# Kernel tuning notes

Measured on AMD Instinct MI355X. Metric: run time of the kernel, lower is better.

## Reference

```python
import jax, jax.numpy as jnp
import numpy as np


def count_sketch(x, h, s, output_dim):
    # x: [B, d], h: [d] int bucket indices, s: [d] +/-1 signs
    # one nonzero per input feature -> scatter-add into output columns
    return jnp.zeros((x.shape[0], output_dim), dtype=x.dtype).at[:, h].add(x * s)


def setup_inputs() -> dict:
    key = jax.random.key(0)
    k1, k2, k3, k4 = jax.random.split(key, 4)
    B, d, D = 2048, 2048, 16000
    img_vec = jax.random.normal(k1, (B, d), dtype=jnp.float32)
    seq_vec = jax.random.normal(k2, (B, d), dtype=jnp.float32)
    h_vec = jax.random.randint(k3, (d,), 0, D, dtype=jnp.int32)
    # random +/-1 signs (count-sketch s vector)
    s_vec = jnp.where(jax.random.bernoulli(k4, 0.5, (d,)), 1.0, -1.0).astype(jnp.float32)
    return {"img_vec": img_vec, "seq_vec": seq_vec, "h_vec": h_vec, "s_vec": s_vec, "output_dim": D}


def reference(img_vec, seq_vec, h_vec, s_vec, output_dim):
    sk_img = count_sketch(img_vec, h_vec, s_vec, output_dim)  # [B, D]
    sk_seq = count_sketch(seq_vec, h_vec, s_vec, output_dim)  # [B, D]
    # circular convolution of the two sketches via FFT (complex64)
    fft_img = jnp.fft.fft(sk_img)
    fft_seq = jnp.fft.fft(sk_seq)
    out = jnp.fft.ifft(fft_img * fft_seq)
    return jnp.real(out).astype(img_vec.dtype)
```

## Files before the change

kernel.cpp:

```cpp
#include <hip/hip_runtime.h>
#include <math.h>

#define NFFT  16000
#define NCCOL 125
#define DFEAT 2048
#define TPB   1024
#define R2OFF 16000
#define R5OFF 16064
#define LDSN  16189

__device__ __forceinline__ float2 cmul(float2 a, float2 b) {
    return make_float2(a.x*b.x - a.y*b.y, a.x*b.y + a.y*b.x);
}
__device__ __forceinline__ float2 cmulc(float2 a, float2 b) {
    return make_float2(a.x*b.x + a.y*b.y, a.y*b.x - a.x*b.y);
}
__device__ __forceinline__ float2 cadd(float2 a, float2 b){ return make_float2(a.x+b.x, a.y+b.y); }
__device__ __forceinline__ float2 csub(float2 a, float2 b){ return make_float2(a.x-b.x, a.y-b.y); }
__device__ __forceinline__ float2 eipi(float a) {
    float s, c;
    sincospif(a, &s, &c);
    return make_float2(c, s);
}

#define C1f 0.30901699437494742f
#define C2f (-0.80901699437494745f)
#define S1f 0.95105651629515357f
#define S2f 0.58778525229247314f

__device__ __forceinline__ void bfly5_fwd(float2& e0, float2& e1, float2& e2,
                                          float2& e3, float2& e4) {
    float2 t1 = cadd(e1, e4), t2 = cadd(e2, e3);
    float2 t3 = csub(e1, e4), t4 = csub(e2, e3);
    float2 f0 = make_float2(e0.x + t1.x + t2.x, e0.y + t1.y + t2.y);
    float2 m1 = make_float2(e0.x + C1f*t1.x + C2f*t2.x, e0.y + C1f*t1.y + C2f*t2.y);
    float2 m2 = make_float2(e0.x + C2f*t1.x + C1f*t2.x, e0.y + C2f*t1.y + C1f*t2.y);
    float2 v1 = make_float2(S1f*t3.x + S2f*t4.x, S1f*t3.y + S2f*t4.y);
    float2 v2 = make_float2(S2f*t3.x - S1f*t4.x, S2f*t3.y - S1f*t4.y);
    e0 = f0;
    e1 = make_float2(m1.x + v1.y, m1.y - v1.x);
    e4 = make_float2(m1.x - v1.y, m1.y + v1.x);
    e2 = make_float2(m2.x + v2.y, m2.y - v2.x);
    e3 = make_float2(m2.x - v2.y, m2.y + v2.x);
}
__device__ __forceinline__ void bfly5_inv(float2& e0, float2& e1, float2& e2,
                                          float2& e3, float2& e4) {
    float2 t1 = cadd(e1, e4), t2 = cadd(e2, e3);
    float2 t3 = csub(e1, e4), t4 = csub(e2, e3);
    float2 f0 = make_float2(e0.x + t1.x + t2.x, e0.y + t1.y + t2.y);
    float2 m1 = make_float2(e0.x + C1f*t1.x + C2f*t2.x, e0.y + C1f*t1.y + C2f*t2.y);
    float2 m2 = make_float2(e0.x + C2f*t1.x + C1f*t2.x, e0.y + C2f*t1.y + C1f*t2.y);
    float2 v1 = make_float2(S1f*t3.x + S2f*t4.x, S1f*t3.y + S2f*t4.y);
    float2 v2 = make_float2(S2f*t3.x - S1f*t4.x, S2f*t3.y - S1f*t4.y);
    e0 = f0;
    e1 = make_float2(m1.x - v1.y, m1.y + v1.x);
    e4 = make_float2(m1.x + v1.y, m1.y - v1.x);
    e2 = make_float2(m2.x - v2.y, m2.y + v2.x);
    e3 = make_float2(m2.x + v2.y, m2.y - v2.x);
}

__global__ void fill_cross_lut(float2* __restrict__ ws) {
    int p = blockIdx.x * 256 + threadIdx.x;
    if (p < NFFT) {
        int r  = p / NCCOL;
        int c  = p - r * NCCOL;
        int k1 = __brev((unsigned)r) >> 25;
        ws[p]  = eipi((float)(c * k1) * (-2.0f / (float)NFFT));
    }
}

__global__ void __launch_bounds__(TPB) __attribute__((amdgpu_waves_per_eu(4, 4)))
mcb_fft_conv_kernel(const float* __restrict__ img, const float* __restrict__ seq,
                    const int* __restrict__ hvec, const float* __restrict__ svec,
                    float* __restrict__ out, const float2* __restrict__ cross)
{
    extern __shared__ float2 buf[];
    const int tid = threadIdx.x;
    const int b   = blockIdx.x;

    #define W2L(k) buf[R2OFF + (k)]
    #define R5L(k) buf[R5OFF + (k)]

    auto CW = [&](int p) -> float2 {
        if (cross) return cross[p];
        int r = p / NCCOL, c = p - r * NCCOL;
        int k1 = __brev((unsigned)r) >> 25;
        return eipi((float)(c * k1) * (-2.0f / (float)NFFT));
    };

    {
        float4* b4 = (float4*)buf;
        for (int p = tid; p < NFFT / 2; p += TPB) b4[p] = make_float4(0.f, 0.f, 0.f, 0.f);
    }
    if (tid < 64) {
        W2L(tid) = eipi(-(float)tid * (1.0f / 64.0f));
    } else if (tid < 64 + 125) {
        int k = tid - 64;
        R5L(k) = eipi((float)k * (-2.0f / 125.0f));
    }
    __syncthreads();

    {
        const float* irow = img + (size_t)b * DFEAT;
        const float* qrow = seq + (size_t)b * DFEAT;
        for (int j = tid; j < DFEAT; j += TPB) {
            float sj = svec[j];
            int   hj = hvec[j];
            atomicAdd(&buf[hj].x, irow[j] * sj);
            atomicAdd(&buf[hj].y, qrow[j] * sj);
        }
    }
    __syncthreads();

    for (int idx = tid; idx < 16 * NCCOL; idx += TPB) {
        const int j = idx / NCCOL;
        const int c = idx - j * NCCOL;
        const int base = j * NCCOL + c;
        float2 x[8];
        #pragma unroll
        for (int t = 0; t < 8; ++t) x[t] = buf[base + 2000 * t];
        #pragma unroll
        for (int t = 0; t < 4; ++t) {
            float2 u = x[t], v = x[t+4];
            x[t]   = cadd(u, v);
            x[t+4] = cmul(csub(u, v), W2L(j + 16*t));
        }
        #pragma unroll
        for (int q = 0; q < 8; q += 4)
            #pragma unroll
            for (int t = 0; t < 2; ++t) {
                float2 u = x[q+t], v = x[q+t+2];
                x[q+t]   = cadd(u, v);
                x[q+t+2] = cmul(csub(u, v), W2L(2*(j + 16*t)));
            }
        {
            float2 w = W2L(4*j);
            #pragma unroll
            for (int q = 0; q < 8; q += 2) {
                float2 u = x[q], v = x[q+1];
                x[q]   = cadd(u, v);
                x[q+1] = cmul(csub(u, v), w);
            }
        }
        #pragma unroll
        for (int t = 0; t < 8; ++t) buf[base + 2000 * t] = x[t];
    }
    __syncthreads();

    for (int idx = tid; idx < 8 * NCCOL; idx += TPB) {
        const int g = idx / NCCOL;
        const int c = idx - g * NCCOL;
        const int base = 2000 * g + c;
        float2 x[16];
        #pragma unroll
        for (int t = 0; t < 16; ++t) x[t] = buf[base + 125 * t];
        #pragma unroll
        for (int t = 0; t < 8; ++t) {
            float2 u = x[t], v = x[t+8];
            x[t]   = cadd(u, v);
            x[t+8] = cmul(csub(u, v), W2L(8*t));
        }
        #pragma unroll
        for (int q = 0; q < 16; q += 8)
            #pragma unroll
            for (int t = 0; t < 4; ++t) {
                float2 u = x[q+t], v = x[q+t+4];
                x[q+t]   = cadd(u, v);
                x[q+t+4] = cmul(csub(u, v), W2L(16*t));
            }
        #pragma unroll
        for (int q = 0; q < 16; q += 4)
            #pragma unroll
            for (int t = 0; t < 2; ++t) {
                float2 u = x[q+t], v = x[q+t+2];
                x[q+t]   = cadd(u, v);
                x[q+t+2] = cmul(csub(u, v), W2L(32*t));
            }
        #pragma unroll
        for (int q = 0; q < 16; q += 2) {
            float2 u = x[q], v = x[q+1];
            x[q]   = cadd(u, v);
            x[q+1] = csub(u, v);
        }
        #pragma unroll
        for (int t = 0; t < 16; ++t)
            buf[base + 125 * t] = cmul(x[t], CW(base + 125 * t));
    }
    __syncthreads();

    for (int idx = tid; idx < 128 * 25; idx += TPB) {
        const int r = idx / 25;
        const int m = idx - r * 25;
        const int base = r * NCCOL + m;
        float2 x0 = buf[base],      x1 = buf[base + 25], x2 = buf[base + 50],
               x3 = buf[base + 75], x4 = buf[base + 100];
        bfly5_fwd(x0, x1, x2, x3, x4);
        x1 = cmul(x1, R5L(m));
        x2 = cmul(x2, R5L(2*m));
        x3 = cmul(x3, R5L(3*m));
        x4 = cmul(x4, R5L(4*m));
        buf[base] = x0; buf[base + 25] = x1; buf[base + 50] = x2;
        buf[base + 75] = x3; buf[base + 100] = x4;
    }
    __syncthreads();

    for (int idx = tid; idx < 128 * 25; idx += TPB) {
        const int r  = idx / 25;
        const int s  = idx - r * 25;
        const int t5 = s / 5;
        const int j2 = s - t5 * 5;
        const int base = r * NCCOL + j2 + 25 * t5;
        float2 x0 = buf[base],      x1 = buf[base + 5],  x2 = buf[base + 10],
               x3 = buf[base + 15], x4 = buf[base + 20];
        bfly5_fwd(x0, x1, x2, x3, x4);
        x1 = cmul(x1, R5L(5*j2));
        x2 = cmul(x2, R5L(10*j2));
        x3 = cmul(x3, R5L(15*j2));
        x4 = cmul(x4, R5L(20*j2));
        buf[base] = x0; buf[base + 5] = x1; buf[base + 10] = x2;
        buf[base + 15] = x3; buf[base + 20] = x4;
    }
    __syncthreads();

    for (int idx = tid; idx < 128 * 25; idx += TPB) {
        const int r = idx / 25;
        const int q = idx - r * 25;
        const int base = r * NCCOL + 5 * q;
        float2 g0 = buf[base], g1 = buf[base+1], g2 = buf[base+2],
               g3 = buf[base+3], g4 = buf[base+4];
        bfly5_fwd(g0, g1, g2, g3, g4);
        g0 = make_float2(g0.x*g0.x - g0.y*g0.y, 2.f*g0.x*g0.y);
        g1 = make_float2(g1.x*g1.x - g1.y*g1.y, 2.f*g1.x*g1.y);
        g2 = make_float2(g2.x*g2.x - g2.y*g2.y, 2.f*g2.x*g2.y);
        g3 = make_float2(g3.x*g3.x - g3.y*g3.y, 2.f*g3.x*g3.y);
        g4 = make_float2(g4.x*g4.x - g4.y*g4.y, 2.f*g4.x*g4.y);
        bfly5_inv(g0, g1, g2, g3, g4);
        buf[base] = g0; buf[base+1] = g1; buf[base+2] = g2;
        buf[base+3] = g3; buf[base+4] = g4;
    }
    __syncthreads();

    for (int idx = tid; idx < 128 * 25; idx += TPB) {
        const int r  = idx / 25;
        const int s  = idx - r * 25;
        const int t5 = s / 5;
        const int j2 = s - t5 * 5;
        const int base = r * NCCOL + j2 + 25 * t5;
        float2 x0 = buf[base],      x1 = buf[base + 5],  x2 = buf[base + 10],
               x3 = buf[base + 15], x4 = buf[base + 20];
        x1 = cmulc(x1, R5L(5*j2));
        x2 = cmulc(x2, R5L(10*j2));
        x3 = cmulc(x3, R5L(15*j2));
        x4 = cmulc(x4, R5L(20*j2));
        bfly5_inv(x0, x1, x2, x3, x4);
        buf[base] = x0; buf[base + 5] = x1; buf[base + 10] = x2;
        buf[base + 15] = x3; buf[base + 20] = x4;
    }
    __syncthreads();

    for (int idx = tid; idx < 128 * 25; idx += TPB) {
        const int r = idx / 25;
        const int m = idx - r * 25;
        const int base = r * NCCOL + m;
        float2 x0 = buf[base],      x1 = buf[base + 25], x2 = buf[base + 50],
               x3 = buf[base + 75], x4 = buf[base + 100];
        x1 = cmulc(x1, R5L(m));
        x2 = cmulc(x2, R5L(2*m));
        x3 = cmulc(x3, R5L(3*m));
        x4 = cmulc(x4, R5L(4*m));
        bfly5_inv(x0, x1, x2, x3, x4);
        buf[base] = x0; buf[base + 25] = x1; buf[base + 50] = x2;
        buf[base + 75] = x3; buf[base + 100] = x4;
    }
    __syncthreads();

    for (int idx = tid; idx < 8 * NCCOL; idx += TPB) {
        const int g = idx / NCCOL;
        const int c = idx - g * NCCOL;
        const int base = 2000 * g + c;
        float2 x[16];
        #pragma unroll
        for (int t = 0; t < 16; ++t)
            x[t] = cmulc(buf[base + 125 * t], CW(base + 125 * t));
        #pragma unroll
        for (int q = 0; q < 16; q += 2) {
            float2 u = x[q], v = x[q+1];
            x[q]   = cadd(u, v);
            x[q+1] = csub(u, v);
        }
        #pragma unroll
        for (int q = 0; q < 16; q += 4)
            #pragma unroll
            for (int t = 0; t < 2; ++t) {
                float2 u = x[q+t];
                float2 v = cmulc(x[q+t+2], W2L(32*t));
                x[q+t]   = cadd(u, v);
                x[q+t+2] = csub(u, v);
            }
        #pragma unroll
        for (int q = 0; q < 16; q += 8)
            #pragma unroll
            for (int t = 0; t < 4; ++t) {
                float2 u = x[q+t];
                float2 v = cmulc(x[q+t+4], W2L(16*t));
                x[q+t]   = cadd(u, v);
                x[q+t+4] = csub(u, v);
            }
        #pragma unroll
        for (int t = 0; t < 8; ++t) {
            float2 u = x[t];
            float2 v = cmulc(x[t+8], W2L(8*t));
            x[t]   = cadd(u, v);
            x[t+8] = csub(u, v);
        }
        #pragma unroll
        for (int t = 0; t < 16; ++t) buf[base + 125 * t] = x[t];
    }
    __syncthreads();

    const float scale = 1.0f / (2.0f * (float)NFFT);
    float* orow = out + (size_t)b * NFFT;
    for (int idx = tid; idx < 16 * NCCOL; idx += TPB) {
        const int j = idx / NCCOL;
        const int c = idx - j * NCCOL;
        const int base = j * NCCOL + c;
        float2 x[8];
        #pragma unroll
        for (int t = 0; t < 8; ++t) x[t] = buf[base + 2000 * t];
        {
            float2 w = W2L(4*j);
            #pragma unroll
            for (int q = 0; q < 8; q += 2) {
                float2 u = x[q];
                float2 v = cmulc(x[q+1], w);
                x[q]   = cadd(u, v);
                x[q+1] = csub(u, v);
            }
        }
        #pragma unroll
        for (int q = 0; q < 8; q += 4)
            #pragma unroll
            for (int t = 0; t < 2; ++t) {
                float2 u = x[q+t];
                float2 v = cmulc(x[q+t+2], W2L(2*(j + 16*t)));
                x[q+t]   = cadd(u, v);
                x[q+t+2] = csub(u, v);
            }
        #pragma unroll
        for (int t = 0; t < 4; ++t) {
            float2 u = x[t];
            float2 v = cmulc(x[t+4], W2L(j + 16*t));
            orow[base + 2000 * t]       = (u.y + v.y) * scale;
            orow[base + 2000 * (t + 4)] = (u.y - v.y) * scale;
        }
    }
}

extern "C" void kernel_launch(void* const* d_in, const int* in_sizes, int n_in,
                              void* d_out, int out_size, void* d_ws, size_t ws_size,
                              hipStream_t stream)
{
    const float* img  = (const float*)d_in[0];
    const float* seq  = (const float*)d_in[1];
    const int*   hvec = (const int*)d_in[2];
    const float* svec = (const float*)d_in[3];
    float* out = (float*)d_out;

    const int B = in_sizes[0] / DFEAT;
    const size_t lds_bytes = (size_t)LDSN * sizeof(float2);

    const bool use_lut = ws_size >= (size_t)NFFT * sizeof(float2);
    float2* cross = use_lut ? (float2*)d_ws : nullptr;
    if (use_lut) {
        hipLaunchKernelGGL(fill_cross_lut, dim3((NFFT + 255) / 256), dim3(256), 0, stream,
                           cross);
    }

    hipFuncSetAttribute((const void*)mcb_fft_conv_kernel,
                        hipFuncAttributeMaxDynamicSharedMemorySize,
                        (int)lds_bytes);

    hipLaunchKernelGGL(mcb_fft_conv_kernel, dim3(B), dim3(TPB), lds_bytes, stream,
                       img, seq, hvec, svec, out, cross);
}
```

Baseline: 371.3 us.

## Pad FFT LDS rows to 132 stride and use power-of-two thread indexing

Changes the shared-memory layout of the 128x125 FFT matrix to a padded row stride of 132, and the cross-twiddle LUT to match. The radix-2 stages now map threads with shifts and masks instead of divisions by 125, run fixed unrolled iteration counts, and the extra padded lanes do dummy work. Scatter-add and output stores are remapped through the padded layout. The aim is to cut integer division cost and change the LDS bank pattern, at the cost of extra LDS footprint (which may affect occupancy) and wasted lanes on padding columns.

```diff
diff --git a/kernel.cpp b/kernel.cpp
--- a/kernel.cpp
+++ b/kernel.cpp
@@ -2,12 +2,15 @@
 #include <math.h>
 
 #define NFFT  16000
+#define NROW  128
 #define NCCOL 125
+#define LDST  132
+#define DATN  (NROW * LDST)
 #define DFEAT 2048
 #define TPB   1024
-#define R2OFF 16000
-#define R5OFF 16064
-#define LDSN  16189
+#define R2OFF DATN
+#define R5OFF (DATN + 64)
+#define LDSN  (DATN + 64 + 125)
 
 __device__ __forceinline__ float2 cmul(float2 a, float2 b) {
     return make_float2(a.x*b.x - a.y*b.y, a.x*b.y + a.y*b.x);
@@ -59,13 +62,17 @@
     e3 = make_float2(m2.x + v2.y, m2.y - v2.x);
 }
 
-__global__ void fill_cross_lut(float2* __restrict__ ws) {
+__global__ void fill_cross_lut_pad(float2* __restrict__ ws) {
     int p = blockIdx.x * 256 + threadIdx.x;
-    if (p < NFFT) {
-        int r  = p / NCCOL;
-        int c  = p - r * NCCOL;
-        int k1 = __brev((unsigned)r) >> 25;
-        ws[p]  = eipi((float)(c * k1) * (-2.0f / (float)NFFT));
+    if (p < DATN) {
+        int r  = p / LDST;
+        int c  = p - r * LDST;
+        float2 v = make_float2(0.f, 0.f);
+        if (c < NCCOL) {
+            int k1 = __brev((unsigned)r) >> 25;
+            v = eipi((float)(c * k1) * (-2.0f / (float)NFFT));
+        }
+        ws[p] = v;
     }
 }
 
@@ -81,16 +88,15 @@
     #define W2L(k) buf[R2OFF + (k)]
     #define R5L(k) buf[R5OFF + (k)]
 
-    auto CW = [&](int p) -> float2 {
-        if (cross) return cross[p];
-        int r = p / NCCOL, c = p - r * NCCOL;
-        int k1 = __brev((unsigned)r) >> 25;
+    auto CW = [&](int row, int c) -> float2 {
+        if (cross) return cross[row * LDST + c];
+        int k1 = __brev((unsigned)row) >> 25;
         return eipi((float)(c * k1) * (-2.0f / (float)NFFT));
     };
 
     {
         float4* b4 = (float4*)buf;
-        for (int p = tid; p < NFFT / 2; p += TPB) b4[p] = make_float4(0.f, 0.f, 0.f, 0.f);
+        for (int p = tid; p < DATN / 2; p += TPB) b4[p] = make_float4(0.f, 0.f, 0.f, 0.f);
     }
     if (tid < 64) {
         W2L(tid) = eipi(-(float)tid * (1.0f / 64.0f));
@@ -103,22 +109,28 @@
     {
         const float* irow = img + (size_t)b * DFEAT;
         const float* qrow = seq + (size_t)b * DFEAT;
-        for (int j = tid; j < DFEAT; j += TPB) {
+        #pragma unroll
+        for (int it = 0; it < DFEAT / TPB; ++it) {
+            const int j = tid + (it << 10);
             float sj = svec[j];
             int   hj = hvec[j];
-            atomicAdd(&buf[hj].x, irow[j] * sj);
-            atomicAdd(&buf[hj].y, qrow[j] * sj);
-        }
-    }
-    __syncthreads();
-
-    for (int idx = tid; idx < 16 * NCCOL; idx += TPB) {
-        const int j = idx / NCCOL;
-        const int c = idx - j * NCCOL;
-        const int base = j * NCCOL + c;
+            int   hr = hj / NCCOL;
+            int   ha = hr * LDST + (hj - hr * NCCOL);
+            atomicAdd(&buf[ha].x, irow[j] * sj);
+            atomicAdd(&buf[ha].y, qrow[j] * sj);
+        }
+    }
+    __syncthreads();
+
+    #pragma unroll
+    for (int it = 0; it < 2; ++it) {
+        const int idx = tid + (it << 10);
+        const int j = idx >> 7;
+        const int c = idx & 127;
+        const int base = j * LDST + c;
         float2 x[8];
         #pragma unroll
-        for (int t = 0; t < 8; ++t) x[t] = buf[base + 2000 * t];
+        for (int t = 0; t < 8; ++t) x[t] = buf[base + 16 * LDST * t];
         #pragma unroll
         for (int t = 0; t < 4; ++t) {
             float2 u = x[t], v = x[t+4];
@@ -143,17 +155,18 @@
             }
         }
         #pragma unroll
-        for (int t = 0; t < 8; ++t) buf[base + 2000 * t] = x[t];
-    }
-    __syncthreads();
-
-    for (int idx = tid; idx < 8 * NCCOL; idx += TPB) {
-        const int g = idx / NCCOL;
-        const int c = idx - g * NCCOL;
-        const int base = 2000 * g + c;
+        for (int t = 0; t < 8; ++t) buf[base + 16 * LDST * t] = x[t];
+    }
+    __syncthreads();
+
+    {
+        const int g = tid >> 7;
+        const int c = tid & 127;
+        const int base = g * (16 * LDST) + c;
+        const int row0 = g << 4;
         float2 x[16];
         #pragma unroll
-        for (int t = 0; t < 16; ++t) x[t] = buf[base + 125 * t];
+        for (int t = 0; t < 16; ++t) x[t] = buf[base + LDST * t];
         #pragma unroll
         for (int t = 0; t < 8; ++t) {
             float2 u = x[t], v = x[t+8];
@@ -184,14 +197,14 @@
         }
         #pragma unroll
         for (int t = 0; t < 16; ++t)
-            buf[base + 125 * t] = cmul(x[t], CW(base + 125 * t));
+            buf[base + LDST * t] = cmul(x[t], CW(row0 + t, c));
     }
     __syncthreads();
 
     for (int idx = tid; idx < 128 * 25; idx += TPB) {
         const int r = idx / 25;
         const int m = idx - r * 25;
-        const int base = r * NCCOL + m;
+        const int base = r * LDST + m;
         float2 x0 = buf[base],      x1 = buf[base + 25], x2 = buf[base + 50],
                x3 = buf[base + 75], x4 = buf[base + 100];
         bfly5_fwd(x0, x1, x2, x3, x4);
@@ -209,7 +222,7 @@
         const int s  = idx - r * 25;
         const int t5 = s / 5;
         const int j2 = s - t5 * 5;
-        const int base = r * NCCOL + j2 + 25 * t5;
+        const int base = r * LDST + j2 + 25 * t5;
         float2 x0 = buf[base],      x1 = buf[base + 5],  x2 = buf[base + 10],
                x3 = buf[base + 15], x4 = buf[base + 20];
         bfly5_fwd(x0, x1, x2, x3, x4);
@@ -225,7 +238,7 @@
     for (int idx = tid; idx < 128 * 25; idx += TPB) {
         const int r = idx / 25;
         const int q = idx - r * 25;
-        const int base = r * NCCOL + 5 * q;
+        const int base = r * LDST + 5 * q;
         float2 g0 = buf[base], g1 = buf[base+1], g2 = buf[base+2],
                g3 = buf[base+3], g4 = buf[base+4];
         bfly5_fwd(g0, g1, g2, g3, g4);
@@ -245,7 +258,7 @@
         const int s  = idx - r * 25;
         const int t5 = s / 5;
         const int j2 = s - t5 * 5;
-        const int base = r * NCCOL + j2 + 25 * t5;
+        const int base = r * LDST + j2 + 25 * t5;
         float2 x0 = buf[base],      x1 = buf[base + 5],  x2 = buf[base + 10],
                x3 = buf[base + 15], x4 = buf[base + 20];
         x1 = cmulc(x1, R5L(5*j2));
@@ -261,7 +274,7 @@
     for (int idx = tid; idx < 128 * 25; idx += TPB) {
         const int r = idx / 25;
         const int m = idx - r * 25;
-        const int base = r * NCCOL + m;
+        const int base = r * LDST + m;
         float2 x0 = buf[base],      x1 = buf[base + 25], x2 = buf[base + 50],
                x3 = buf[base + 75], x4 = buf[base + 100];
         x1 = cmulc(x1, R5L(m));
@@ -274,14 +287,15 @@
     }
     __syncthreads();
 
-    for (int idx = tid; idx < 8 * NCCOL; idx += TPB) {
-        const int g = idx / NCCOL;
-        const int c = idx - g * NCCOL;
-        const int base = 2000 * g + c;
+    {
+        const int g = tid >> 7;
+        const int c = tid & 127;
+        const int base = g * (16 * LDST) + c;
+        const int row0 = g << 4;
         float2 x[16];
         #pragma unroll
         for (int t = 0; t < 16; ++t)
-            x[t] = cmulc(buf[base + 125 * t], CW(base + 125 * t));
+            x[t] = cmulc(buf[base + LDST * t], CW(row0 + t, c));
         #pragma unroll
         for (int q = 0; q < 16; q += 2) {
             float2 u = x[q], v = x[q+1];
@@ -314,19 +328,21 @@
             x[t+8] = csub(u, v);
         }
         #pragma unroll
-        for (int t = 0; t < 16; ++t) buf[base + 125 * t] = x[t];
+        for (int t = 0; t < 16; ++t) buf[base + LDST * t] = x[t];
     }
     __syncthreads();
 
     const float scale = 1.0f / (2.0f * (float)NFFT);
     float* orow = out + (size_t)b * NFFT;
-    for (int idx = tid; idx < 16 * NCCOL; idx += TPB) {
-        const int j = idx / NCCOL;
-        const int c = idx - j * NCCOL;
-        const int base = j * NCCOL + c;
+    #pragma unroll
+    for (int it = 0; it < 2; ++it) {
+        const int idx = tid + (it << 10);
+        const int j = idx >> 7;
+        const int c = idx & 127;
+        const int base = j * LDST + c;
         float2 x[8];
         #pragma unroll
-        for (int t = 0; t < 8; ++t) x[t] = buf[base + 2000 * t];
+        for (int t = 0; t < 8; ++t) x[t] = buf[base + 16 * LDST * t];
         {
             float2 w = W2L(4*j);
             #pragma unroll
@@ -346,12 +362,21 @@
                 x[q+t]   = cadd(u, v);
                 x[q+t+2] = csub(u, v);
             }
+        float ylo[4], yhi[4];
         #pragma unroll
         for (int t = 0; t < 4; ++t) {
             float2 u = x[t];
             float2 v = cmulc(x[t+4], W2L(j + 16*t));
-            orow[base + 2000 * t]       = (u.y + v.y) * scale;
-            orow[base + 2000 * (t + 4)] = (u.y - v.y) * scale;
+            ylo[t] = (u.y + v.y) * scale;
+            yhi[t] = (u.y - v.y) * scale;
+        }
+        if (c < NCCOL) {
+            const int gbase = j * NCCOL + c;
+            #pragma unroll
+            for (int t = 0; t < 4; ++t) {
+                orow[gbase + 2000 * t]       = ylo[t];
+                orow[gbase + 2000 * (t + 4)] = yhi[t];
+            }
         }
     }
 }
@@ -369,11 +394,11 @@
     const int B = in_sizes[0] / DFEAT;
     const size_t lds_bytes = (size_t)LDSN * sizeof(float2);
 
-    const bool use_lut = ws_size >= (size_t)NFFT * sizeof(float2);
+    const bool use_lut = ws_size >= (size_t)DATN * sizeof(float2);
     float2* cross = use_lut ? (float2*)d_ws : nullptr;
     if (use_lut) {
-        hipLaunchKernelGGL(fill_cross_lut, dim3((NFFT + 255) / 256), dim3(256), 0, stream,
-                           cross);
+        hipLaunchKernelGGL(fill_cross_lut_pad, dim3((DATN + 255) / 256), dim3(256), 0,
+                           stream, cross);
     }
 
     hipFuncSetAttribute((const void*)mcb_fft_conv_kernel,
```

Result: no change. 377.0 us (+1.5%).

## Restructure FFT stages so each wave owns 8 rows, removing block barriers

Applied to the files above, without the earlier changes.

The radix-2 decomposition is regrouped into a 16-point first stage (stride 1000) and an 8-point second stage, so each wavefront owns 8 contiguous rows of 125 columns. All radix-8, radix-5, pointwise-square and inverse stages for those rows then run inside a single wave, with no __syncthreads between them. This removes about seven block-wide barriers per FFT. In exchange, lanes sit idle in the 125- and 200-item wave loops, only 1000 of 1024 threads work in the outer stages, and register pressure rises with 16-element arrays.

```diff
diff --git a/kernel.cpp b/kernel.cpp
--- a/kernel.cpp
+++ b/kernel.cpp
@@ -81,10 +81,9 @@
     #define W2L(k) buf[R2OFF + (k)]
     #define R5L(k) buf[R5OFF + (k)]
 
-    auto CW = [&](int p) -> float2 {
-        if (cross) return cross[p];
-        int r = p / NCCOL, c = p - r * NCCOL;
-        int k1 = __brev((unsigned)r) >> 25;
+    auto CW = [&](int row, int c) -> float2 {
+        if (cross) return cross[row * NCCOL + c];
+        int k1 = __brev((unsigned)row) >> 25;
         return eipi((float)(c * k1) * (-2.0f / (float)NFFT));
     };
 
@@ -103,7 +102,9 @@
     {
         const float* irow = img + (size_t)b * DFEAT;
         const float* qrow = seq + (size_t)b * DFEAT;
-        for (int j = tid; j < DFEAT; j += TPB) {
+        #pragma unroll
+        for (int it = 0; it < DFEAT / TPB; ++it) {
+            const int j = tid + (it << 10);
             float sj = svec[j];
             int   hj = hvec[j];
             atomicAdd(&buf[hj].x, irow[j] * sj);
@@ -112,225 +113,213 @@
     }
     __syncthreads();
 
-    for (int idx = tid; idx < 16 * NCCOL; idx += TPB) {
-        const int j = idx / NCCOL;
-        const int c = idx - j * NCCOL;
+    if (tid < 8 * NCCOL) {
+        const int j = tid / NCCOL;
+        const int c = tid - j * NCCOL;
         const int base = j * NCCOL + c;
-        float2 x[8];
-        #pragma unroll
-        for (int t = 0; t < 8; ++t) x[t] = buf[base + 2000 * t];
-        #pragma unroll
-        for (int t = 0; t < 4; ++t) {
-            float2 u = x[t], v = x[t+4];
+        float2 x[16];
+        #pragma unroll
+        for (int t = 0; t < 16; ++t) x[t] = buf[base + 1000 * t];
+        #pragma unroll
+        for (int t = 0; t < 8; ++t) {
+            float2 u = x[t], v = x[t+8];
             x[t]   = cadd(u, v);
-            x[t+4] = cmul(csub(u, v), W2L(j + 16*t));
-        }
-        #pragma unroll
-        for (int q = 0; q < 8; q += 4)
+            x[t+8] = cmul(csub(u, v), W2L(j + 8*t));
+        }
+        #pragma unroll
+        for (int q = 0; q < 16; q += 8)
+            #pragma unroll
+            for (int t = 0; t < 4; ++t) {
+                float2 u = x[q+t], v = x[q+t+4];
+                x[q+t]   = cadd(u, v);
+                x[q+t+4] = cmul(csub(u, v), W2L(2*(j + 8*t)));
+            }
+        #pragma unroll
+        for (int q = 0; q < 16; q += 4)
             #pragma unroll
             for (int t = 0; t < 2; ++t) {
                 float2 u = x[q+t], v = x[q+t+2];
                 x[q+t]   = cadd(u, v);
-                x[q+t+2] = cmul(csub(u, v), W2L(2*(j + 16*t)));
+                x[q+t+2] = cmul(csub(u, v), W2L(4*(j + 8*t)));
             }
         {
-            float2 w = W2L(4*j);
+            float2 w = W2L(8*j);
+            #pragma unroll
+            for (int q = 0; q < 16; q += 2) {
+                float2 u = x[q], v = x[q+1];
+                x[q]   = cadd(u, v);
+                x[q+1] = cmul(csub(u, v), w);
+            }
+        }
+        #pragma unroll
+        for (int t = 0; t < 16; ++t) buf[base + 1000 * t] = x[t];
+    }
+    __syncthreads();
+
+    {
+        const int wv = tid >> 6;
+        const int ln = tid & 63;
+        const int rbase = wv * 8 * NCCOL;
+        const int row0 = wv << 3;
+
+        for (int c = ln; c < NCCOL; c += 64) {
+            const int base = rbase + c;
+            float2 x[8];
+            #pragma unroll
+            for (int t = 0; t < 8; ++t) x[t] = buf[base + NCCOL * t];
+            #pragma unroll
+            for (int t = 0; t < 4; ++t) {
+                float2 u = x[t], v = x[t+4];
+                x[t]   = cadd(u, v);
+                x[t+4] = cmul(csub(u, v), W2L(16*t));
+            }
+            #pragma unroll
+            for (int q = 0; q < 8; q += 4)
+                #pragma unroll
+                for (int t = 0; t < 2; ++t) {
+                    float2 u = x[q+t], v = x[q+t+2];
+                    x[q+t]   = cadd(u, v);
+                    x[q+t+2] = cmul(csub(u, v), W2L(32*t));
+                }
             #pragma unroll
             for (int q = 0; q < 8; q += 2) {
                 float2 u = x[q], v = x[q+1];
                 x[q]   = cadd(u, v);
-                x[q+1] = cmul(csub(u, v), w);
-            }
-        }
-        #pragma unroll
-        for (int t = 0; t < 8; ++t) buf[base + 2000 * t] = x[t];
-    }
-    __syncthreads();
-
-    for (int idx = tid; idx < 8 * NCCOL; idx += TPB) {
-        const int g = idx / NCCOL;
-        const int c = idx - g * NCCOL;
-        const int base = 2000 * g + c;
-        float2 x[16];
-        #pragma unroll
-        for (int t = 0; t < 16; ++t) x[t] = buf[base + 125 * t];
-        #pragma unroll
-        for (int t = 0; t < 8; ++t) {
-            float2 u = x[t], v = x[t+8];
-            x[t]   = cadd(u, v);
-            x[t+8] = cmul(csub(u, v), W2L(8*t));
-        }
-        #pragma unroll
-        for (int q = 0; q < 16; q += 8)
+                x[q+1] = csub(u, v);
+            }
+            #pragma unroll
+            for (int t = 0; t < 8; ++t)
+                buf[base + NCCOL * t] = cmul(x[t], CW(row0 + t, c));
+        }
+
+        for (int idx = ln; idx < 200; idx += 64) {
+            const int rl = idx / 25;
+            const int m  = idx - rl * 25;
+            const int base = rbase + rl * NCCOL + m;
+            float2 x0 = buf[base],      x1 = buf[base + 25], x2 = buf[base + 50],
+                   x3 = buf[base + 75], x4 = buf[base + 100];
+            bfly5_fwd(x0, x1, x2, x3, x4);
+            x1 = cmul(x1, R5L(m));
+            x2 = cmul(x2, R5L(2*m));
+            x3 = cmul(x3, R5L(3*m));
+            x4 = cmul(x4, R5L(4*m));
+            buf[base] = x0; buf[base + 25] = x1; buf[base + 50] = x2;
+            buf[base + 75] = x3; buf[base + 100] = x4;
+        }
+
+        for (int idx = ln; idx < 200; idx += 64) {
+            const int rl = idx / 25;
+            const int s  = idx - rl * 25;
+            const int t5 = s / 5;
+            const int j2 = s - t5 * 5;
+            const int base = rbase + rl * NCCOL + j2 + 25 * t5;
+            float2 x0 = buf[base],      x1 = buf[base + 5],  x2 = buf[base + 10],
+                   x3 = buf[base + 15], x4 = buf[base + 20];
+            bfly5_fwd(x0, x1, x2, x3, x4);
+            x1 = cmul(x1, R5L(5*j2));
+            x2 = cmul(x2, R5L(10*j2));
+            x3 = cmul(x3, R5L(15*j2));
+            x4 = cmul(x4, R5L(20*j2));
+            buf[base] = x0; buf[base + 5] = x1; buf[base + 10] = x2;
+            buf[base + 15] = x3; buf[base + 20] = x4;
+        }
+
+        for (int idx = ln; idx < 200; idx += 64) {
+            const int rl = idx / 25;
+            const int q  = idx - rl * 25;
+            const int base = rbase + rl * NCCOL + 5 * q;
+            float2 g0 = buf[base], g1 = buf[base+1], g2 = buf[base+2],
+                   g3 = buf[base+3], g4 = buf[base+4];
+            bfly5_fwd(g0, g1, g2, g3, g4);
+            g0 = make_float2(g0.x*g0.x - g0.y*g0.y, 2.f*g0.x*g0.y);
+            g1 = make_float2(g1.x*g1.x - g1.y*g1.y, 2.f*g1.x*g1.y);
+            g2 = make_float2(g2.x*g2.x - g2.y*g2.y, 2.f*g2.x*g2.y);
+            g3 = make_float2(g3.x*g3.x - g3.y*g3.y, 2.f*g3.x*g3.y);
+            g4 = make_float2(g4.x*g4.x - g4.y*g4.y, 2.f*g4.x*g4.y);
+            bfly5_inv(g0, g1, g2, g3, g4);
+            buf[base] = g0; buf[base+1] = g1; buf[base+2] = g2;
+            buf[base+3] = g3; buf[base+4] = g4;
+        }
+
+        for (int idx = ln; idx < 200; idx += 64) {
+            const int rl = idx / 25;
+            const int s  = idx - rl * 25;
+            const int t5 = s / 5;
+            const int j2 = s - t5 * 5;
+            const int base = rbase + rl * NCCOL + j2 + 25 * t5;
+            float2 x0 = buf[base],      x1 = buf[base + 5],  x2 = buf[base + 10],
+                   x3 = buf[base + 15], x4 = buf[base + 20];
+            x1 = cmulc(x1, R5L(5*j2));
+            x2 = cmulc(x2, R5L(10*j2));
+            x3 = cmulc(x3, R5L(15*j2));
+            x4 = cmulc(x4, R5L(20*j2));
+            bfly5_inv(x0, x1, x2, x3, x4);
+            buf[base] = x0; buf[base + 5] = x1; buf[base + 10] = x2;
+            buf[base + 15] = x3; buf[base + 20] = x4;
+        }
+
+        for (int idx = ln; idx < 200; idx += 64) {
+            const int rl = idx / 25;
+            const int m  = idx - rl * 25;
+            const int base = rbase + rl * NCCOL + m;
+            float2 x0 = buf[base],      x1 = buf[base + 25], x2 = buf[base + 50],
+                   x3 = buf[base + 75], x4 = buf[base + 100];
+            x1 = cmulc(x1, R5L(m));
+            x2 = cmulc(x2, R5L(2*m));
+            x3 = cmulc(x3, R5L(3*m));
+            x4 = cmulc(x4, R5L(4*m));
+            bfly5_inv(x0, x1, x2, x3, x4);
+            buf[base] = x0; buf[base + 25] = x1; buf[base + 50] = x2;
+            buf[base + 75] = x3; buf[base + 100] = x4;
+        }
+
+        for (int c = ln; c < NCCOL; c += 64) {
+            const int base = rbase + c;
+            float2 x[8];
+            #pragma unroll
+            for (int t = 0; t < 8; ++t)
+                x[t] = cmulc(buf[base + NCCOL * t], CW(row0 + t, c));
+            #pragma unroll
+            for (int q = 0; q < 8; q += 2) {
+                float2 u = x[q], v = x[q+1];
+                x[q]   = cadd(u, v);
+                x[q+1] = csub(u, v);
+            }
+            #pragma unroll
+            for (int q = 0; q < 8; q += 4)
+                #pragma unroll
+                for (int t = 0; t < 2; ++t) {
+                    float2 u = x[q+t];
+                    float2 v = cmulc(x[q+t+2], W2L(32*t));
+                    x[q+t]   = cadd(u, v);
+                    x[q+t+2] = csub(u, v);
+                }
             #pragma unroll
             for (int t = 0; t < 4; ++t) {
-                float2 u = x[q+t], v = x[q+t+4];
-                x[q+t]   = cadd(u, v);
-                x[q+t+4] = cmul(csub(u, v), W2L(16*t));
-            }
-        #pragma unroll
-        for (int q = 0; q < 16; q += 4)
-            #pragma unroll
-            for (int t = 0; t < 2; ++t) {
-                float2 u = x[q+t], v = x[q+t+2];
-                x[q+t]   = cadd(u, v);
-                x[q+t+2] = cmul(csub(u, v), W2L(32*t));
-            }
-        #pragma unroll
-        for (int q = 0; q < 16; q += 2) {
-            float2 u = x[q], v = x[q+1];
-            x[q]   = cadd(u, v);
-            x[q+1] = csub(u, v);
-        }
-        #pragma unroll
-        for (int t = 0; t < 16; ++t)
-            buf[base + 125 * t] = cmul(x[t], CW(base + 125 * t));
-    }
-    __syncthreads();
-
-    for (int idx = tid; idx < 128 * 25; idx += TPB) {
-        const int r = idx / 25;
-        const int m = idx - r * 25;
-        const int base = r * NCCOL + m;
-        float2 x0 = buf[base],      x1 = buf[base + 25], x2 = buf[base + 50],
-               x3 = buf[base + 75], x4 = buf[base + 100];
-        bfly5_fwd(x0, x1, x2, x3, x4);
-        x1 = cmul(x1, R5L(m));
-        x2 = cmul(x2, R5L(2*m));
-        x3 = cmul(x3, R5L(3*m));
-        x4 = cmul(x4, R5L(4*m));
-        buf[base] = x0; buf[base + 25] = x1; buf[base + 50] = x2;
-        buf[base + 75] = x3; buf[base + 100] = x4;
-    }
-    __syncthreads();
-
-    for (int idx = tid; idx < 128 * 25; idx += TPB) {
-        const int r  = idx / 25;
-        const int s  = idx - r * 25;
-        const int t5 = s / 5;
-        const int j2 = s - t5 * 5;
-        const int base = r * NCCOL + j2 + 25 * t5;
-        float2 x0 = buf[base],      x1 = buf[base + 5],  x2 = buf[base + 10],
-               x3 = buf[base + 15], x4 = buf[base + 20];
-        bfly5_fwd(x0, x1, x2, x3, x4);
-        x1 = cmul(x1, R5L(5*j2));
-        x2 = cmul(x2, R5L(10*j2));
-        x3 = cmul(x3, R5L(15*j2));
-        x4 = cmul(x4, R5L(20*j2));
-        buf[base] = x0; buf[base + 5] = x1; buf[base + 10] = x2;
-        buf[base + 15] = x3; buf[base + 20] = x4;
-    }
-    __syncthreads();
-
-    for (int idx = tid; idx < 128 * 25; idx += TPB) {
-        const int r = idx / 25;
-        const int q = idx - r * 25;
-        const int base = r * NCCOL + 5 * q;
-        float2 g0 = buf[base], g1 = buf[base+1], g2 = buf[base+2],
-               g3 = buf[base+3], g4 = buf[base+4];
-        bfly5_fwd(g0, g1, g2, g3, g4);
-        g0 = make_float2(g0.x*g0.x - g0.y*g0.y, 2.f*g0.x*g0.y);
-        g1 = make_float2(g1.x*g1.x - g1.y*g1.y, 2.f*g1.x*g1.y);
-        g2 = make_float2(g2.x*g2.x - g2.y*g2.y, 2.f*g2.x*g2.y);
-        g3 = make_float2(g3.x*g3.x - g3.y*g3.y, 2.f*g3.x*g3.y);
-        g4 = make_float2(g4.x*g4.x - g4.y*g4.y, 2.f*g4.x*g4.y);
-        bfly5_inv(g0, g1, g2, g3, g4);
-        buf[base] = g0; buf[base+1] = g1; buf[base+2] = g2;
-        buf[base+3] = g3; buf[base+4] = g4;
-    }
-    __syncthreads();
-
-    for (int idx = tid; idx < 128 * 25; idx += TPB) {
-        const int r  = idx / 25;
-        const int s  = idx - r * 25;
-        const int t5 = s / 5;
-        const int j2 = s - t5 * 5;
-        const int base = r * NCCOL + j2 + 25 * t5;
-        float2 x0 = buf[base],      x1 = buf[base + 5],  x2 = buf[base + 10],
-               x3 = buf[base + 15], x4 = buf[base + 20];
-        x1 = cmulc(x1, R5L(5*j2));
-        x2 = cmulc(x2, R5L(10*j2));
-        x3 = cmulc(x3, R5L(15*j2));
-        x4 = cmulc(x4, R5L(20*j2));
-        bfly5_inv(x0, x1, x2, x3, x4);
-        buf[base] = x0; buf[base + 5] = x1; buf[base + 10] = x2;
-        buf[base + 15] = x3; buf[base + 20] = x4;
-    }
-    __syncthreads();
-
-    for (int idx = tid; idx < 128 * 25; idx += TPB) {
-        const int r = idx / 25;
-        const int m = idx - r * 25;
-        const int base = r * NCCOL + m;
-        float2 x0 = buf[base],      x1 = buf[base + 25], x2 = buf[base + 50],
-               x3 = buf[base + 75], x4 = buf[base + 100];
-        x1 = cmulc(x1, R5L(m));
-        x2 = cmulc(x2, R5L(2*m));
-        x3 = cmulc(x3, R5L(3*m));
-        x4 = cmulc(x4, R5L(4*m));
-        bfly5_inv(x0, x1, x2, x3, x4);
-        buf[base] = x0; buf[base + 25] = x1; buf[base + 50] = x2;
-        buf[base + 75] = x3; buf[base + 100] = x4;
-    }
-    __syncthreads();
-
-    for (int idx = tid; idx < 8 * NCCOL; idx += TPB) {
-        const int g = idx / NCCOL;
-        const int c = idx - g * NCCOL;
-        const int base = 2000 * g + c;
-        float2 x[16];
-        #pragma unroll
-        for (int t = 0; t < 16; ++t)
-            x[t] = cmulc(buf[base + 125 * t], CW(base + 125 * t));
-        #pragma unroll
-        for (int q = 0; q < 16; q += 2) {
-            float2 u = x[q], v = x[q+1];
-            x[q]   = cadd(u, v);
-            x[q+1] = csub(u, v);
-        }
-        #pragma unroll
-        for (int q = 0; q < 16; q += 4)
-            #pragma unroll
-            for (int t = 0; t < 2; ++t) {
-                float2 u = x[q+t];
-                float2 v = cmulc(x[q+t+2], W2L(32*t));
-                x[q+t]   = cadd(u, v);
-                x[q+t+2] = csub(u, v);
-            }
-        #pragma unroll
-        for (int q = 0; q < 16; q += 8)
-            #pragma unroll
-            for (int t = 0; t < 4; ++t) {
-                float2 u = x[q+t];
-                float2 v = cmulc(x[q+t+4], W2L(16*t));
-                x[q+t]   = cadd(u, v);
-                x[q+t+4] = csub(u, v);
-            }
-        #pragma unroll
-        for (int t = 0; t < 8; ++t) {
-            float2 u = x[t];
-            float2 v = cmulc(x[t+8], W2L(8*t));
-            x[t]   = cadd(u, v);
-            x[t+8] = csub(u, v);
-        }
-        #pragma unroll
-        for (int t = 0; t < 16; ++t) buf[base + 125 * t] = x[t];
+                float2 u = x[t];
+                float2 v = cmulc(x[t+4], W2L(16*t));
+                x[t]   = cadd(u, v);
+                x[t+4] = csub(u, v);
+            }
+            #pragma unroll
+            for (int t = 0; t < 8; ++t) buf[base + NCCOL * t] = x[t];
+        }
     }
     __syncthreads();
 
     const float scale = 1.0f / (2.0f * (float)NFFT);
     float* orow = out + (size_t)b * NFFT;
-    for (int idx = tid; idx < 16 * NCCOL; idx += TPB) {
-        const int j = idx / NCCOL;
-        const int c = idx - j * NCCOL;
+    if (tid < 8 * NCCOL) {
+        const int j = tid / NCCOL;
+        const int c = tid - j * NCCOL;
         const int base = j * NCCOL + c;
-        float2 x[8];
-        #pragma unroll
-        for (int t = 0; t < 8; ++t) x[t] = buf[base + 2000 * t];
+        float2 x[16];
+        #pragma unroll
+        for (int t = 0; t < 16; ++t) x[t] = buf[base + 1000 * t];
         {
-            float2 w = W2L(4*j);
-            #pragma unroll
-            for (int q = 0; q < 8; q += 2) {
+            float2 w = W2L(8*j);
+            #pragma unroll
+            for (int q = 0; q < 16; q += 2) {
                 float2 u = x[q];
                 float2 v = cmulc(x[q+1], w);
                 x[q]   = cadd(u, v);
@@ -338,20 +327,29 @@
             }
         }
         #pragma unroll
-        for (int q = 0; q < 8; q += 4)
+        for (int q = 0; q < 16; q += 4)
             #pragma unroll
             for (int t = 0; t < 2; ++t) {
                 float2 u = x[q+t];
-                float2 v = cmulc(x[q+t+2], W2L(2*(j + 16*t)));
+                float2 v = cmulc(x[q+t+2], W2L(4*(j + 8*t)));
                 x[q+t]   = cadd(u, v);
                 x[q+t+2] = csub(u, v);
             }
         #pragma unroll
-        for (int t = 0; t < 4; ++t) {
+        for (int q = 0; q < 16; q += 8)
+            #pragma unroll
+            for (int t = 0; t < 4; ++t) {
+                float2 u = x[q+t];
+                float2 v = cmulc(x[q+t+4], W2L(2*(j + 8*t)));
+                x[q+t]   = cadd(u, v);
+                x[q+t+4] = csub(u, v);
+            }
+        #pragma unroll
+        for (int t = 0; t < 8; ++t) {
             float2 u = x[t];
-            float2 v = cmulc(x[t+4], W2L(j + 16*t));
-            orow[base + 2000 * t]       = (u.y + v.y) * scale;
-            orow[base + 2000 * (t + 4)] = (u.y - v.y) * scale;
+            float2 v = cmulc(x[t+8], W2L(j + 8*t));
+            orow[base + 1000 * t]        = (u.y + v.y) * scale;
+            orow[base + 1000 * t + 8000] = (u.y - v.y) * scale;
         }
     }
 }
```

Result: slower. 379.4 us (+2.2%).
